# Kernel optimization log

Measured on AMD Instinct MI355X. Metric: run time of the kernel, lower is better.

## Reference

```python
import jax, jax.numpy as jnp
import numpy as np

VOCAB = 8192  # upper bound on integer values appearing in features


def setup_inputs() -> dict:
    key = jax.random.key(0)
    # [B, L] integer codes; each row is treated as a SET of values (duplicates ignored)
    features = jax.random.randint(key, (4096, 256), 0, VOCAB, dtype=jnp.int32)
    return {"features": features}


def reference(features) -> jnp.ndarray:
    # np.intersect1d / np.union1d compute set intersection/union of unique values.
    # Equivalent vectorized form: binary presence matrix P[i, v] = 1 iff value v in row i.
    B, L = features.shape
    rows = jnp.arange(B)[:, None]                                  # [B, 1]
    presence = jnp.zeros((B, VOCAB), jnp.float32).at[rows, features].set(1.0)  # [B, V]
    inter = presence @ presence.T                                  # [B, B] |A_i & A_j|
    sizes = presence.sum(axis=1)                                   # [B]    |A_i|
    union = sizes[:, None] + sizes[None, :] - inter                # [B, B] |A_i | A_j|
    # original returns -intersection/union (note the negation), 0 when union == 0
    sim = jnp.where(union != 0, -inter / jnp.where(union != 0, union, 1.0), 0.0)
    return sim
```

## Files before the change

kernel.cpp:

```cpp
#include <hip/hip_runtime.h>
#include <hip/hip_bf16.h>
#include <stdint.h>

#define B_ROWS 4096
#define L_FEAT 256
#define VOCAB  8192

#define BM 128
#define BN 128
#define BK 64
#define NSTEP (VOCAB / BK)

typedef __attribute__((ext_vector_type(4))) int   intx4;
typedef __attribute__((ext_vector_type(4))) float floatx4;

__device__ __forceinline__ void async_copy16(const void* gsrc, void* ldst) {
  __builtin_amdgcn_global_load_lds(
      (const __attribute__((address_space(1))) void*)gsrc,
      (__attribute__((address_space(3))) void*)ldst, 16, 0, 0);
}

__global__ __launch_bounds__(256) void presence_kernel(
    const int* __restrict__ f,
    unsigned char* __restrict__ P,
    float* __restrict__ sizes) {
  __shared__ __align__(16) unsigned char row_p[VOCAB];
  const int row = blockIdx.x;
  const int tid = threadIdx.x;

  uint4* rp4 = (uint4*)row_p;
  const uint4 z = make_uint4(0u, 0u, 0u, 0u);
  #pragma unroll
  for (int j = 0; j < 2; ++j) rp4[tid + j * 256] = z;
  __syncthreads();

  const int v = f[row * L_FEAT + tid];
  row_p[v] = 1;
  __syncthreads();

  int cnt = 0;
  uint4* op4 = (uint4*)(P + (size_t)row * VOCAB);
  #pragma unroll
  for (int j = 0; j < 2; ++j) {
    const uint4 x = rp4[tid + j * 256];
    op4[tid + j * 256] = x;
    cnt += __popc(x.x) + __popc(x.y) + __popc(x.z) + __popc(x.w);
  }
  #pragma unroll
  for (int off = 32; off > 0; off >>= 1) cnt += __shfl_down(cnt, off);
  __shared__ int ws[4];
  if ((tid & 63) == 0) ws[tid >> 6] = cnt;
  __syncthreads();
  if (tid == 0) sizes[row] = (float)(ws[0] + ws[1] + ws[2] + ws[3]);
}

__global__ __launch_bounds__(256) void gemm_kernel(
    const unsigned char* __restrict__ P,
    const float* __restrict__ sizes,
    float* __restrict__ out) {
  int bid = blockIdx.x;
  bid = (bid & 7) * 66 + (bid >> 3);
  int b = bid, by = 0, rem = 32;
  while (b >= rem) { b -= rem; ++by; --rem; }
  const int bx = by + b;
  const int iBase = by * BM;
  const int jBase = bx * BN;

  __shared__ __align__(16) unsigned char As[3][BM * BK];
  __shared__ __align__(16) unsigned char Bs[3][BN * BK];

  const int tid  = threadIdx.x;
  const int wave = tid >> 6, lane = tid & 63;
  const int wm = wave >> 1, wn = wave & 1;
  const int col16 = lane & 15, quad = lane >> 4;

  intx4 acc[4][4];
  #pragma unroll
  for (int a = 0; a < 4; ++a)
    #pragma unroll
    for (int c = 0; c < 4; ++c) acc[a][c] = (intx4){0, 0, 0, 0};

  const int srow = lane >> 2;
  const int scol = ((lane & 3) ^ ((lane >> 3) & 3)) * 16;

  #define STAGE(buf, k0)                                                      \
    {                                                                         \
      _Pragma("unroll")                                                       \
      for (int t = 0; t < 2; ++t) {                                           \
        const int c = wave + t * 4;                           \
        const int r = c * 16 + srow;                     \
        async_copy16(P + (size_t)(iBase + r) * VOCAB + (k0) + scol,           \
                     &As[buf][c * 1024]);                                     \
        async_copy16(P + (size_t)(jBase + r) * VOCAB + (k0) + scol,           \
                     &Bs[buf][c * 1024]);                                     \
      }                                                                       \
    }

  STAGE(0, 0);
  STAGE(1, BK);

  const int sw = (col16 >> 1) & 3;

  int cur = 0, pre = 2;
  for (int i = 0; i < NSTEP; ++i) {
    asm volatile("s_waitcnt vmcnt(4)" ::: "memory");
    __builtin_amdgcn_s_barrier();

    const int kpre = ((i + 2) * BK) & (VOCAB - 1);
    STAGE(pre, kpre);

    const unsigned char* Ab = As[cur];
    const unsigned char* Bb = Bs[cur];
    intx4 a[4], bfr[4];
    #pragma unroll
    for (int tm = 0; tm < 4; ++tm)
      a[tm] = *(const intx4*)&Ab[(wm * 64 + tm * 16 + col16) * BK +
                                 (quad ^ sw) * 16];
    #pragma unroll
    for (int tn = 0; tn < 4; ++tn)
      bfr[tn] = *(const intx4*)&Bb[(wn * 64 + tn * 16 + col16) * BK +
                                   (quad ^ sw) * 16];

    __builtin_amdgcn_s_setprio(1);
    #pragma unroll
    for (int tm = 0; tm < 4; ++tm)
      #pragma unroll
      for (int tn = 0; tn < 4; ++tn)
        acc[tm][tn] = __builtin_amdgcn_mfma_i32_16x16x64_i8(
            a[tm], bfr[tn], acc[tm][tn], 0, 0, 0);
    __builtin_amdgcn_s_setprio(0);

    cur = (cur == 2) ? 0 : cur + 1;
    pre = (pre == 2) ? 0 : pre + 1;
  }

  #pragma unroll
  for (int tm = 0; tm < 4; ++tm) {
    const int rowb = iBase + wm * 64 + tm * 16 + quad * 4;
    const float si0 = sizes[rowb + 0], si1 = sizes[rowb + 1];
    const float si2 = sizes[rowb + 2], si3 = sizes[rowb + 3];
    #pragma unroll
    for (int tn = 0; tn < 4; ++tn) {
      const int col = jBase + wn * 64 + tn * 16 + col16;
      const float sj = sizes[col];
      floatx4 tv;
      {
        const float inter = (float)acc[tm][tn][0];
        const float u = si0 + sj - inter;
        tv[0] = (u != 0.f) ? (-inter / u) : 0.f;
      }
      {
        const float inter = (float)acc[tm][tn][1];
        const float u = si1 + sj - inter;
        tv[1] = (u != 0.f) ? (-inter / u) : 0.f;
      }
      {
        const float inter = (float)acc[tm][tn][2];
        const float u = si2 + sj - inter;
        tv[2] = (u != 0.f) ? (-inter / u) : 0.f;
      }
      {
        const float inter = (float)acc[tm][tn][3];
        const float u = si3 + sj - inter;
        tv[3] = (u != 0.f) ? (-inter / u) : 0.f;
      }
      __builtin_nontemporal_store(tv[0], &out[(size_t)(rowb + 0) * B_ROWS + col]);
      __builtin_nontemporal_store(tv[1], &out[(size_t)(rowb + 1) * B_ROWS + col]);
      __builtin_nontemporal_store(tv[2], &out[(size_t)(rowb + 2) * B_ROWS + col]);
      __builtin_nontemporal_store(tv[3], &out[(size_t)(rowb + 3) * B_ROWS + col]);
      __builtin_nontemporal_store(tv, (floatx4*)&out[(size_t)col * B_ROWS + rowb]);
    }
  }
}

extern "C" void kernel_launch(void* const* d_in, const int* in_sizes, int n_in,
                              void* d_out, int out_size, void* d_ws, size_t ws_size,
                              hipStream_t stream) {
  const int* features = (const int*)d_in[0];
  float* out = (float*)d_out;
  unsigned char* P = (unsigned char*)d_ws;
  float* sizes = (float*)((char*)d_ws + (size_t)B_ROWS * VOCAB);

  presence_kernel<<<B_ROWS, 256, 0, stream>>>(features, P, sizes);
  gemm_kernel<<<528, 256, 0, stream>>>(P, sizes, out);
}
```

Baseline: 181.6 us.

## Pack presence matrix as FP4 nibbles and use scaled FP4 MFMA

Switches the presence matrix from one byte per vocabulary entry to 4-bit FP4 (value 1.0 encoded as 0x2) per entry, halving the bytes produced by the presence kernel and streamed by the GEMM. The GEMM now uses the MI355 scaled f8f6f4 32x32x64 MFMA in FP4 mode with float accumulation. Tiles are restructured so each wave loads contiguous 32-row slabs, and the epilogue is adapted to the 32x32 output layout. The aim is to cut global and LDS traffic and use higher-throughput low-precision matrix instructions, at the cost of relying on exact FP4 encoding and the operand-layout assumptions of the scaled MFMA.

```diff
diff --git a/kernel.cpp b/kernel.cpp
--- a/kernel.cpp
+++ b/kernel.cpp
@@ -1,18 +1,20 @@
 #include <hip/hip_runtime.h>
-#include <hip/hip_bf16.h>
 #include <stdint.h>
 
 #define B_ROWS 4096
 #define L_FEAT 256
 #define VOCAB  8192
-
+#define ROWB   (VOCAB / 2)
 #define BM 128
 #define BN 128
-#define BK 64
-#define NSTEP (VOCAB / BK)
+#define BKE 64
+#define BKB 32
+#define NSTEP (VOCAB / BKE)
 
-typedef __attribute__((ext_vector_type(4))) int   intx4;
-typedef __attribute__((ext_vector_type(4))) float floatx4;
+typedef __attribute__((ext_vector_type(4)))  int   intx4;
+typedef __attribute__((ext_vector_type(8)))  int   intx8;
+typedef __attribute__((ext_vector_type(4)))  float floatx4;
+typedef __attribute__((ext_vector_type(16))) float floatx16;
 
 __device__ __forceinline__ void async_copy16(const void* gsrc, void* ldst) {
   __builtin_amdgcn_global_load_lds(
@@ -22,30 +24,24 @@
 
 __global__ __launch_bounds__(256) void presence_kernel(
     const int* __restrict__ f,
-    unsigned char* __restrict__ P,
+    uint32_t* __restrict__ P,
     float* __restrict__ sizes) {
-  __shared__ __align__(16) unsigned char row_p[VOCAB];
+  __shared__ uint32_t rw[VOCAB / 8];
   const int row = blockIdx.x;
   const int tid = threadIdx.x;
 
-  uint4* rp4 = (uint4*)row_p;
-  const uint4 z = make_uint4(0u, 0u, 0u, 0u);
   #pragma unroll
-  for (int j = 0; j < 2; ++j) rp4[tid + j * 256] = z;
+  for (int j = 0; j < 4; ++j) rw[tid + j * 256] = 0u;
   __syncthreads();
 
   const int v = f[row * L_FEAT + tid];
-  row_p[v] = 1;
+  atomicOr(&rw[v >> 3], 0x2u << ((v & 7) * 4));
   __syncthreads();
 
-  int cnt = 0;
-  uint4* op4 = (uint4*)(P + (size_t)row * VOCAB);
-  #pragma unroll
-  for (int j = 0; j < 2; ++j) {
-    const uint4 x = rp4[tid + j * 256];
-    op4[tid + j * 256] = x;
-    cnt += __popc(x.x) + __popc(x.y) + __popc(x.z) + __popc(x.w);
-  }
+  const uint4 x = ((const uint4*)rw)[tid];
+  ((uint4*)(P + (size_t)row * (ROWB / 4)))[tid] = x;
+  int cnt = __popc(x.x & 0x22222222u) + __popc(x.y & 0x22222222u) +
+            __popc(x.z & 0x22222222u) + __popc(x.w & 0x22222222u);
   #pragma unroll
   for (int off = 32; off > 0; off >>= 1) cnt += __shfl_down(cnt, off);
   __shared__ int ws[4];
@@ -66,68 +62,69 @@
   const int iBase = by * BM;
   const int jBase = bx * BN;
 
-  __shared__ __align__(16) unsigned char As[3][BM * BK];
-  __shared__ __align__(16) unsigned char Bs[3][BN * BK];
+  __shared__ __align__(16) unsigned char As[3][4096];
+  __shared__ __align__(16) unsigned char Bs[3][4096];
 
   const int tid  = threadIdx.x;
   const int wave = tid >> 6, lane = tid & 63;
   const int wm = wave >> 1, wn = wave & 1;
-  const int col16 = lane & 15, quad = lane >> 4;
+  const int r31 = lane & 31, khalf = lane >> 5;
 
-  intx4 acc[4][4];
+  floatx16 acc[2][2];
   #pragma unroll
-  for (int a = 0; a < 4; ++a)
+  for (int ai = 0; ai < 2; ++ai)
     #pragma unroll
-    for (int c = 0; c < 4; ++c) acc[a][c] = (intx4){0, 0, 0, 0};
+    for (int ci = 0; ci < 2; ++ci)
+      #pragma unroll
+      for (int e = 0; e < 16; ++e) acc[ai][ci][e] = 0.f;
 
-  const int srow = lane >> 2;
-  const int scol = ((lane & 3) ^ ((lane >> 3) & 3)) * 16;
+  const unsigned char* srcA =
+      P + (size_t)(iBase + wave * 32 + r31) * ROWB + khalf * 16;
+  const unsigned char* srcB =
+      P + (size_t)(jBase + wave * 32 + r31) * ROWB + khalf * 16;
 
-  #define STAGE(buf, k0)                                                      \
+  #define STAGE(buf, k0b)                                                     \
     {                                                                         \
-      _Pragma("unroll")                                                       \
-      for (int t = 0; t < 2; ++t) {                                           \
-        const int c = wave + t * 4;                           \
-        const int r = c * 16 + srow;                     \
-        async_copy16(P + (size_t)(iBase + r) * VOCAB + (k0) + scol,           \
-                     &As[buf][c * 1024]);                                     \
-        async_copy16(P + (size_t)(jBase + r) * VOCAB + (k0) + scol,           \
-                     &Bs[buf][c * 1024]);                                     \
-      }                                                                       \
+      async_copy16(srcA + (k0b), &As[buf][wave * 1024]);                      \
+      async_copy16(srcB + (k0b), &Bs[buf][wave * 1024]);                      \
     }
 
   STAGE(0, 0);
-  STAGE(1, BK);
-
-  const int sw = (col16 >> 1) & 3;
+  STAGE(1, BKB);
 
   int cur = 0, pre = 2;
   for (int i = 0; i < NSTEP; ++i) {
-    asm volatile("s_waitcnt vmcnt(4)" ::: "memory");
+    asm volatile("s_waitcnt vmcnt(2)" ::: "memory");
     __builtin_amdgcn_s_barrier();
 
-    const int kpre = ((i + 2) * BK) & (VOCAB - 1);
-    STAGE(pre, kpre);
+    STAGE(pre, ((i + 2) * BKB) & (ROWB - 1));
 
-    const unsigned char* Ab = As[cur];
-    const unsigned char* Bb = Bs[cur];
-    intx4 a[4], bfr[4];
+    intx4 a4[2], b4[2];
     #pragma unroll
-    for (int tm = 0; tm < 4; ++tm)
-      a[tm] = *(const intx4*)&Ab[(wm * 64 + tm * 16 + col16) * BK +
-                                 (quad ^ sw) * 16];
+    for (int t = 0; t < 2; ++t) {
+      a4[t] = *(const intx4*)&As[cur][(wm * 2 + t) * 1024 + lane * 16];
+      b4[t] = *(const intx4*)&Bs[cur][(wn * 2 + t) * 1024 + lane * 16];
+    }
+    intx8 a8[2], b8[2];
     #pragma unroll
-    for (int tn = 0; tn < 4; ++tn)
-      bfr[tn] = *(const intx4*)&Bb[(wn * 64 + tn * 16 + col16) * BK +
-                                   (quad ^ sw) * 16];
+    for (int t = 0; t < 2; ++t) {
+      #pragma unroll
+      for (int e = 0; e < 4; ++e) {
+        a8[t][e] = a4[t][e];  a8[t][e + 4] = 0;
+        b8[t][e] = b4[t][e];  b8[t][e + 4] = 0;
+      }
+    }
 
     __builtin_amdgcn_s_setprio(1);
     #pragma unroll
-    for (int tm = 0; tm < 4; ++tm)
+    for (int tm = 0; tm < 2; ++tm)
       #pragma unroll
-      for (int tn = 0; tn < 4; ++tn)
-        acc[tm][tn] = __builtin_amdgcn_mfma_i32_16x16x64_i8(
-            a[tm], bfr[tn], acc[tm][tn], 0, 0, 0);
+      for (int tn = 0; tn < 2; ++tn)
+        acc[tm][tn] = __builtin_amdgcn_mfma_scale_f32_32x32x64_f8f6f4(
+            a8[tm], b8[tn], acc[tm][tn],
+            4, 4,
+            0, 127,
+            0, 127);
     __builtin_amdgcn_s_setprio(0);
 
     cur = (cur == 2) ? 0 : cur + 1;
@@ -135,40 +132,28 @@
   }
 
   #pragma unroll
-  for (int tm = 0; tm < 4; ++tm) {
-    const int rowb = iBase + wm * 64 + tm * 16 + quad * 4;
-    const float si0 = sizes[rowb + 0], si1 = sizes[rowb + 1];
-    const float si2 = sizes[rowb + 2], si3 = sizes[rowb + 3];
+  for (int tm = 0; tm < 2; ++tm) {
+    const int rowb = iBase + wm * 64 + tm * 32 + 4 * khalf;
     #pragma unroll
-    for (int tn = 0; tn < 4; ++tn) {
-      const int col = jBase + wn * 64 + tn * 16 + col16;
-      const float sj = sizes[col];
-      floatx4 tv;
-      {
-        const float inter = (float)acc[tm][tn][0];
-        const float u = si0 + sj - inter;
-        tv[0] = (u != 0.f) ? (-inter / u) : 0.f;
+    for (int tn = 0; tn < 2; ++tn) {
+      const int colb = jBase + wn * 64 + tn * 32 + r31;
+      const float sj = sizes[colb];
+      #pragma unroll
+      for (int q = 0; q < 4; ++q) {
+        const int rq = rowb + 8 * q;
+        floatx4 tv;
+        #pragma unroll
+        for (int j = 0; j < 4; ++j) {
+          const float inter = acc[tm][tn][4 * q + j];
+          const float u = sizes[rq + j] + sj - inter;
+          tv[j] = (u != 0.f) ? (-inter / u) : 0.f;
+        }
+        __builtin_nontemporal_store(tv[0], &out[(size_t)(rq + 0) * B_ROWS + colb]);
+        __builtin_nontemporal_store(tv[1], &out[(size_t)(rq + 1) * B_ROWS + colb]);
+        __builtin_nontemporal_store(tv[2], &out[(size_t)(rq + 2) * B_ROWS + colb]);
+        __builtin_nontemporal_store(tv[3], &out[(size_t)(rq + 3) * B_ROWS + colb]);
+        __builtin_nontemporal_store(tv, (floatx4*)&out[(size_t)colb * B_ROWS + rq]);
       }
-      {
-        const float inter = (float)acc[tm][tn][1];
-        const float u = si1 + sj - inter;
-        tv[1] = (u != 0.f) ? (-inter / u) : 0.f;
-      }
-      {
-        const float inter = (float)acc[tm][tn][2];
-        const float u = si2 + sj - inter;
-        tv[2] = (u != 0.f) ? (-inter / u) : 0.f;
-      }
-      {
-        const float inter = (float)acc[tm][tn][3];
-        const float u = si3 + sj - inter;
-        tv[3] = (u != 0.f) ? (-inter / u) : 0.f;
-      }
-      __builtin_nontemporal_store(tv[0], &out[(size_t)(rowb + 0) * B_ROWS + col]);
-      __builtin_nontemporal_store(tv[1], &out[(size_t)(rowb + 1) * B_ROWS + col]);
-      __builtin_nontemporal_store(tv[2], &out[(size_t)(rowb + 2) * B_ROWS + col]);
-      __builtin_nontemporal_store(tv[3], &out[(size_t)(rowb + 3) * B_ROWS + col]);
-      __builtin_nontemporal_store(tv, (floatx4*)&out[(size_t)col * B_ROWS + rowb]);
     }
   }
 }
@@ -178,9 +163,9 @@
                               hipStream_t stream) {
   const int* features = (const int*)d_in[0];
   float* out = (float*)d_out;
-  unsigned char* P = (unsigned char*)d_ws;
-  float* sizes = (float*)((char*)d_ws + (size_t)B_ROWS * VOCAB);
+  uint32_t* P = (uint32_t*)d_ws;
+  float* sizes = (float*)((char*)d_ws + (size_t)B_ROWS * ROWB);
 
   presence_kernel<<<B_ROWS, 256, 0, stream>>>(features, P, sizes);
-  gemm_kernel<<<528, 256, 0, stream>>>(P, sizes, out);
+  gemm_kernel<<<528, 256, 0, stream>>>((const unsigned char*)P, sizes, out);
 }
```

Result: slower. 248.8 us (+37.0%).
